# Optimization experiments

Hardware: AMD Instinct MI355X
Metric: run time of the kernel (lower is better)

## Reference

```python
import jax, jax.numpy as jnp
import numpy as np

B, N, C = 256, 196, 256
RES, RES_, STRIDE = 14, 7, 2
H, KD, D = 16, 16, 64          # heads, key_dim, d=attn_ratio*key_dim
NH_KD, DH = H * KD, H * D      # 256, 1024
HW = DH + NH_KD                # kv width 1280
OUT = 512
EPS = 1e-5
SCALE = KD ** -0.5


def make_bias_idxs():
    pts = [(i, j) for i in range(RES) for j in range(RES)]
    pts_ = [(i, j) for i in range(RES_) for j in range(RES_)]
    offsets, idxs = {}, []
    for p1 in pts_:
        for p2 in pts:
            off = (abs(p1[0] * STRIDE - p2[0]), abs(p1[1] * STRIDE - p2[1]))
            if off not in offsets:
                offsets[off] = len(offsets)
            idxs.append(offsets[off])
    return np.array(idxs, np.int32).reshape(len(pts_), len(pts)), len(offsets)


def bn(x, g, b, m, v):
    return (x - m) * (g / jnp.sqrt(v + EPS)) + b


def hardswish(x):
    return x * jnp.clip(x + 3.0, 0.0, 6.0) / 6.0


def setup_inputs() -> dict:
    key = jax.random.key(0)
    ks = jax.random.split(key, 12)
    idxs, n_off = make_bias_idxs()
    s_in, s_dh = (2.0 / C) ** 0.5, (2.0 / DH) ** 0.5
    return {
        "x": jax.random.normal(ks[0], (B, N, C), jnp.float32),
        "W_kv": jax.random.normal(ks[1], (HW, C), jnp.float32) * s_in,
        "g_kv": jnp.ones((HW,)), "b_kv": jnp.zeros((HW,)),
        "m_kv": jax.random.normal(ks[2], (HW,)) * 0.1,
        "v_kv": jax.random.uniform(ks[3], (HW,), minval=0.5, maxval=1.5),
        "W_q": jax.random.normal(ks[4], (NH_KD, C), jnp.float32) * s_in,
        "g_q": jnp.ones((NH_KD,)), "b_q": jnp.zeros((NH_KD,)),
        "m_q": jax.random.normal(ks[5], (NH_KD,)) * 0.1,
        "v_q": jax.random.uniform(ks[6], (NH_KD,), minval=0.5, maxval=1.5),
        "W_p": jax.random.normal(ks[7], (OUT, DH), jnp.float32) * s_dh,
        "g_p": jnp.ones((OUT,)), "b_p": jnp.zeros((OUT,)),
        "m_p": jax.random.normal(ks[8], (OUT,)) * 0.1,
        "v_p": jax.random.uniform(ks[9], (OUT,), minval=0.5, maxval=1.5),
        "attn_biases": jax.random.normal(ks[10], (H, n_off), jnp.float32) * 0.02,
        "bias_idxs": jnp.asarray(idxs),
    }


def reference(x, W_kv, g_kv, b_kv, m_kv, v_kv, W_q, g_q, b_q, m_q, v_q,
              W_p, g_p, b_p, m_p, v_p, attn_biases, bias_idxs):
    # kv branch: Linear(no bias) + BN over flattened tokens
    kv = bn(jnp.einsum('bnc,hc->bnh', x, W_kv), g_kv, b_kv, m_kv, v_kv)
    kv = kv.reshape(B, N, H, KD + D)
    k, v = kv[..., :KD], kv[..., KD:]                 # [B,N,H,KD], [B,N,H,D]
    # q branch: spatial subsample stride 2 then LinearNorm
    xs = x.reshape(B, RES, RES, C)[:, ::STRIDE, ::STRIDE].reshape(B, RES_ * RES_, C)
    q = bn(jnp.einsum('bnc,hc->bnh', xs, W_q), g_q, b_q, m_q, v_q)
    q = q.reshape(B, RES_ * RES_, H, KD)              # [B,49,H,KD]
    bias = attn_biases[:, bias_idxs]                  # [H,49,196]
    attn = jnp.einsum('bqhd,bkhd->bhqk', q, k) * SCALE + bias
    attn = jax.nn.softmax(attn, axis=-1)
    o = jnp.einsum('bhqk,bkhd->bqhd', attn, v).reshape(B, RES_ * RES_, DH)
    return bn(jnp.einsum('bnd,od->bno', hardswish(o), W_p), g_p, b_p, m_p, v_p)
```

## Files before the change

kernel.cpp:

```cpp
#include <hip/hip_runtime.h>

typedef unsigned short u16;
typedef unsigned int u32;
typedef __attribute__((ext_vector_type(8))) short bf16x8;
typedef __attribute__((ext_vector_type(4))) float f32x4;

__device__ __forceinline__ u16 f2bf(float x) {
  union { float f; u32 u; } un; un.f = x;
  u32 r = un.u + 0x7FFFu + ((un.u >> 16) & 1u);
  return (u16)(r >> 16);
}

__device__ __forceinline__ void gl_lds16(const u16* gsrc, u16* ldst) {
  __builtin_amdgcn_global_load_lds(
      (const __attribute__((address_space(1))) void*)gsrc,
      (__attribute__((address_space(3))) void*)ldst,
      16, 0, 0);
}

__global__ __launch_bounds__(256) void prep_misc(
    const float* __restrict__ Wkv, const float* __restrict__ Wq, const float* __restrict__ Wp,
    const float* __restrict__ gkv, const float* __restrict__ bkv, const float* __restrict__ mkv, const float* __restrict__ vkv,
    const float* __restrict__ gq, const float* __restrict__ bq, const float* __restrict__ mq, const float* __restrict__ vq,
    const float* __restrict__ gp, const float* __restrict__ bp, const float* __restrict__ mp, const float* __restrict__ vp,
    const float* __restrict__ ab, const int* __restrict__ bidx,
    u16* __restrict__ wkvb, u16* __restrict__ wqb, u16* __restrict__ wpb,
    float* __restrict__ skv, float* __restrict__ tkv,
    float* __restrict__ sq, float* __restrict__ tq,
    float* __restrict__ sp, float* __restrict__ tp,
    float* __restrict__ biasf)
{
  int i = blockIdx.x * 256 + threadIdx.x;
  if (i < 327680) { wkvb[i] = f2bf(Wkv[i]); return; }
  i -= 327680;
  if (i < 65536) { wqb[i] = f2bf(Wq[i]); return; }
  i -= 65536;
  if (i < 524288) { wpb[i] = f2bf(Wp[i]); return; }
  i -= 524288;
  if (i < 153664) { biasf[i] = ab[(i / 9604) * 196 + bidx[i % 9604]]; return; }
  i -= 153664;
  if (i < 1280) { float s = gkv[i] * rsqrtf(vkv[i] + 1e-5f); skv[i] = s; tkv[i] = bkv[i] - mkv[i] * s; return; }
  i -= 1280;
  if (i < 256) { float s = gq[i] * rsqrtf(vq[i] + 1e-5f); sq[i] = s * 0.25f; tq[i] = (bq[i] - mq[i] * s) * 0.25f; return; }
  i -= 256;
  if (i < 512) { float s = gp[i] * rsqrtf(vp[i] + 1e-5f); sp[i] = s; tp[i] = bp[i] - mp[i] * s; return; }
}

__global__ __launch_bounds__(256) void conv_x(const float* __restrict__ x, u16* __restrict__ xb)
{
  int u = blockIdx.x * 256 + threadIdx.x;
  float4 v = ((const float4*)x)[u];
  uint2 o;
  o.x = (u32)f2bf(v.x) | ((u32)f2bf(v.y) << 16);
  o.y = (u32)f2bf(v.z) | ((u32)f2bf(v.w) << 16);
  ((uint2*)xb)[u] = o;
}

__global__ __launch_bounds__(256) void gemm_bn(
    const u16* __restrict__ A, const u16* __restrict__ W,
    const float* __restrict__ sv, const float* __restrict__ tv,
    float* __restrict__ outp, int N, int K, int NBLK)
{
  __shared__ u16 As[128 * 64];
  __shared__ u16 Bs[128 * 64];
  const int tid = threadIdx.x;
  const int lane = tid & 63;
  const int wv = tid >> 6, wr = wv >> 1, wc = wv & 1;
  const int lo = lane & 15, hi = lane >> 4;

  int bid = blockIdx.x;
  int cpx = gridDim.x >> 3;
  int wg = (bid & 7) * cpx + (bid >> 3);
  const int m0 = (wg / NBLK) * 128, n0 = (wg % NBLK) * 128;

  f32x4 zero4 = {0.f, 0.f, 0.f, 0.f};
  f32x4 acc[4][4];
#pragma unroll
  for (int m = 0; m < 4; ++m)
#pragma unroll
    for (int n = 0; n < 4; ++n) acc[m][n] = zero4;

  for (int kt = 0; kt < K; kt += 64) {
    __syncthreads();
#pragma unroll
    for (int i = 0; i < 4; ++i) {
      int e = (i * 256 + tid) * 8;
      int r = e >> 6, c = e & 63;
      int cs = c ^ ((r & 7) << 3);
      gl_lds16(A + (long)(m0 + r) * K + (kt + cs), As + e);
      gl_lds16(W + (long)(n0 + r) * K + (kt + cs), Bs + e);
    }
    __syncthreads();
#pragma unroll
    for (int kk = 0; kk < 64; kk += 32) {
      bf16x8 af[4], bfr[4];
#pragma unroll
      for (int m = 0; m < 4; ++m)
        af[m] = *(const bf16x8*)(As + (wr * 64 + m * 16 + lo) * 64 + ((kk + hi * 8) ^ ((lo & 7) << 3)));
#pragma unroll
      for (int n = 0; n < 4; ++n)
        bfr[n] = *(const bf16x8*)(Bs + (wc * 64 + n * 16 + lo) * 64 + ((kk + hi * 8) ^ ((lo & 7) << 3)));
#pragma unroll
      for (int m = 0; m < 4; ++m)
#pragma unroll
        for (int n = 0; n < 4; ++n)
          acc[m][n] = __builtin_amdgcn_mfma_f32_16x16x32_bf16(af[m], bfr[n], acc[m][n], 0, 0, 0);
    }
  }
#pragma unroll
  for (int m = 0; m < 4; ++m) {
    const int row0 = m0 + wr * 64 + m * 16 + hi * 4;
#pragma unroll
    for (int n = 0; n < 4; ++n) {
      const int col = n0 + wc * 64 + n * 16 + lo;
      const float s = sv[col], t = tv[col];
#pragma unroll
      for (int j = 0; j < 4; ++j)
        outp[(long)(row0 + j) * N + col] = acc[m][n][j] * s + t;
    }
  }
}

#define WOFF  13312
#define VTS   208
#define KOFF  13312
#define KS    24
#define QOFF  18304
#define QS    24
#define POFF  13312
#define PS    208
#define SMEM_N 26624

__device__ __forceinline__ int swz(int col, int rowkey) {
  return (col < 192) ? (col ^ ((rowkey & 7) << 3)) : col;
}

__global__ __launch_bounds__(256, 3) void fused_attn(
    const u16* __restrict__ xb, const u16* __restrict__ wkvb, const u16* __restrict__ wqb,
    const float* __restrict__ skv, const float* __restrict__ tkv,
    const float* __restrict__ sqv, const float* __restrict__ tqv,
    const float* __restrict__ biasf, u16* __restrict__ osw)
{
  __shared__ __align__(16) u16 sm[SMEM_N];
  const int tid = threadIdx.x;
  const int bid = blockIdx.x;
  const int wg = (bid & 7) * 512 + (bid >> 3);
  const int bb = wg >> 4, hh = wg & 15;
  const int w = tid >> 6, lane = tid & 63, lo = lane & 15, hi = lane >> 4;

  const u16* xbase = xb + (long)bb * 196 * 256;
  const u16* wkvh = wkvb + (long)hh * 80 * 256;
  const u16* wqh  = wqb + (long)hh * 16 * 256;

  const int NM = (w == 0) ? 4 : 3;
  f32x4 z4 = {0.f, 0.f, 0.f, 0.f};
  f32x4 acc[4][5];
#pragma unroll
  for (int u = 0; u < 4; ++u)
#pragma unroll
    for (int nf = 0; nf < 5; ++nf) acc[u][nf] = z4;
  f32x4 qacc = z4;

  int qi = w * 16 + lo; if (qi > 48) qi = 48;
  const int gr = (qi / 7) * 28 + (qi % 7) * 2;

  for (int kt = 0; kt < 256; kt += 64) {
    __syncthreads();
#pragma unroll
    for (int i = 0; i < 7; ++i) {
      if (i < 6 || tid < 128) {
        int e = (i * 256 + tid) * 8;
        int r = e >> 6, c = e & 63;
        int xr = (r < 196) ? r : 195;
        int cs = c ^ ((r & 7) << 3);
        gl_lds16(xbase + (long)xr * 256 + kt + cs, sm + e);
      }
    }
#pragma unroll
    for (int i = 0; i < 3; ++i) {
      int e = (i * 256 + tid) * 8;
      int r = e >> 6, c = e & 63;
      int cs = c ^ ((r & 7) << 3);
      const u16* src = (r < 80) ? (wkvh + (long)r * 256 + kt + cs)
                                : (wqh + (long)(r - 80) * 256 + kt + cs);
      gl_lds16(src, sm + WOFF + e);
    }
    __syncthreads();
    __builtin_amdgcn_s_setprio(1);
#pragma unroll
    for (int kk = 0; kk < 64; kk += 32) {
      bf16x8 bfr[6];
#pragma unroll
      for (int nf = 0; nf < 6; ++nf)
        bfr[nf] = *(const bf16x8*)(sm + WOFF + (nf * 16 + lo) * 64 + ((kk + hi * 8) ^ ((lo & 7) << 3)));
      {
        bf16x8 aqf = *(const bf16x8*)(sm + gr * 64 + ((kk + hi * 8) ^ ((gr & 7) << 3)));
        qacc = __builtin_amdgcn_mfma_f32_16x16x32_bf16(aqf, bfr[5], qacc, 0, 0, 0);
      }
#pragma unroll
      for (int u = 0; u < 4; ++u) {
        if (u < NM) {
          const int mf = w + u * 4;
          bf16x8 af = *(const bf16x8*)(sm + (mf * 16 + lo) * 64 + ((kk + hi * 8) ^ ((lo & 7) << 3)));
#pragma unroll
          for (int nf = 0; nf < 5; ++nf)
            acc[u][nf] = __builtin_amdgcn_mfma_f32_16x16x32_bf16(af, bfr[nf], acc[u][nf], 0, 0, 0);
        }
      }
    }
    __builtin_amdgcn_s_setprio(0);
  }
  __syncthreads();

#pragma unroll
  for (int u = 0; u < 4; ++u) {
    if (u < NM) {
      const int mf = w + u * 4;
#pragma unroll
      for (int nf = 0; nf < 5; ++nf) {
        const int col = nf * 16 + lo;
        const float s = skv[hh * 80 + col], t = tkv[hh * 80 + col];
#pragma unroll
        for (int j = 0; j < 4; ++j) {
          const int nn = mf * 16 + hi * 4 + j;
          const u16 bv = f2bf(acc[u][nf][j] * s + t);
          if (col < 16) sm[KOFF + nn * KS + col] = bv;
          else          sm[(col - 16) * VTS + swz(nn, col - 16)] = bv;
        }
      }
    }
  }
  {
    const float s = sqv[hh * 16 + lo], t = tqv[hh * 16 + lo];
#pragma unroll
    for (int j = 0; j < 4; ++j) {
      const int r = w * 16 + hi * 4 + j;
      sm[QOFF + r * QS + lo] = f2bf(qacc[j] * s + t);
    }
  }
  __syncthreads();

  f32x4 sc[13];
  {
    bf16x8 zf = {0, 0, 0, 0, 0, 0, 0, 0};
    bf16x8 aq2 = zf;
    if (hi < 2) aq2 = *(const bf16x8*)(sm + QOFF + (w * 16 + lo) * QS + hi * 8);
#pragma unroll
    for (int t13 = 0; t13 < 13; ++t13) {
      bf16x8 bk = zf;
      if (hi < 2) bk = *(const bf16x8*)(sm + KOFF + (t13 * 16 + lo) * KS + hi * 8);
      sc[t13] = __builtin_amdgcn_mfma_f32_16x16x32_bf16(aq2, bk, z4, 0, 0, 0);
    }
  }
  __syncthreads();

  float rs[4];
#pragma unroll
  for (int j = 0; j < 4; ++j) {
    const int row = w * 16 + hi * 4 + j;
    const int rb = (row < 49) ? row : 0;
    float vals[13];
#pragma unroll
    for (int t = 0; t < 13; ++t) {
      const int col = t * 16 + lo;
      vals[t] = (col < 196) ? sc[t][j] + biasf[(hh * 49 + rb) * 196 + col] : -1e30f;
    }
    float mx = vals[0];
#pragma unroll
    for (int t = 1; t < 13; ++t) mx = fmaxf(mx, vals[t]);
#pragma unroll
    for (int s = 1; s < 16; s <<= 1) mx = fmaxf(mx, __shfl_xor(mx, s, 64));
    float sum = 0.f;
#pragma unroll
    for (int t = 0; t < 13; ++t) { float p = __expf(vals[t] - mx); vals[t] = p; sum += p; }
#pragma unroll
    for (int s = 1; s < 16; s <<= 1) sum += __shfl_xor(sum, s, 64);
#pragma unroll
    for (int t = 0; t < 13; ++t) sm[POFF + row * PS + swz(t * 16 + lo, row)] = f2bf(vals[t]);
    rs[j] = sum;
  }

  f32x4 oacc[4];
#pragma unroll
  for (int n = 0; n < 4; ++n) oacc[n] = z4;
  __builtin_amdgcn_s_setprio(1);
#pragma unroll
  for (int kt = 0; kt < 192; kt += 32) {
    bf16x8 ap = *(const bf16x8*)(sm + POFF + (w * 16 + lo) * PS + ((kt + hi * 8) ^ ((lo & 7) << 3)));
#pragma unroll
    for (int n = 0; n < 4; ++n) {
      bf16x8 bv = *(const bf16x8*)(sm + (n * 16 + lo) * VTS + ((kt + hi * 8) ^ ((lo & 7) << 3)));
      oacc[n] = __builtin_amdgcn_mfma_f32_16x16x32_bf16(ap, bv, oacc[n], 0, 0, 0);
    }
  }
  {
    bf16x8 zf = {0, 0, 0, 0, 0, 0, 0, 0};
    bf16x8 ap = zf;
    if (hi < 2) ap = *(const bf16x8*)(sm + POFF + (w * 16 + lo) * PS + 192 + hi * 8);
#pragma unroll
    for (int n = 0; n < 4; ++n) {
      bf16x8 bv = zf;
      if (hi < 2) bv = *(const bf16x8*)(sm + (n * 16 + lo) * VTS + 192 + hi * 8);
      oacc[n] = __builtin_amdgcn_mfma_f32_16x16x32_bf16(ap, bv, oacc[n], 0, 0, 0);
    }
  }
  __builtin_amdgcn_s_setprio(0);

#pragma unroll
  for (int j = 0; j < 4; ++j) {
    const int row = w * 16 + hi * 4 + j;
    if (row < 49) {
      const float rinv = 1.f / rs[j];
      const long ob = ((long)(bb * 49 + row)) * 1024 + hh * 64 + lo;
#pragma unroll
      for (int n = 0; n < 4; ++n) {
        float val = oacc[n][j] * rinv;
        float hs = val * fminf(fmaxf(val + 3.f, 0.f), 6.f) * (1.f / 6.f);
        osw[ob + n * 16] = f2bf(hs);
      }
    }
  }
}

extern "C" void kernel_launch(void* const* d_in, const int* in_sizes, int n_in,
                              void* d_out, int out_size, void* d_ws, size_t ws_size,
                              hipStream_t stream)
{
  const float* x   = (const float*)d_in[0];
  const float* Wkv = (const float*)d_in[1];
  const float* gkv = (const float*)d_in[2];
  const float* bkv = (const float*)d_in[3];
  const float* mkv = (const float*)d_in[4];
  const float* vkv = (const float*)d_in[5];
  const float* Wq  = (const float*)d_in[6];
  const float* gq  = (const float*)d_in[7];
  const float* bq  = (const float*)d_in[8];
  const float* mq  = (const float*)d_in[9];
  const float* vq  = (const float*)d_in[10];
  const float* Wp  = (const float*)d_in[11];
  const float* gp  = (const float*)d_in[12];
  const float* bp  = (const float*)d_in[13];
  const float* mp  = (const float*)d_in[14];
  const float* vp  = (const float*)d_in[15];
  const float* ab  = (const float*)d_in[16];
  const int* bidx  = (const int*)d_in[17];

  char* ws = (char*)d_ws;
  size_t off = 0;
  auto alloc = [&](size_t bytes) -> char* {
    char* p = ws + off;
    off += (bytes + 255) & ~(size_t)255;
    return p;
  };
  u16* x_bf   = (u16*)alloc((size_t)50176 * 256 * 2);
  u16* wkv_bf = (u16*)alloc((size_t)1280 * 256 * 2);
  u16* wq_bf  = (u16*)alloc((size_t)256 * 256 * 2);
  u16* wp_bf  = (u16*)alloc((size_t)512 * 1024 * 2);
  u16* hsw    = (u16*)alloc((size_t)12544 * 1024 * 2);
  float* bias_f = (float*)alloc((size_t)153664 * 4);
  float* s_kv = (float*)alloc(1280 * 4);
  float* t_kv = (float*)alloc(1280 * 4);
  float* s_q  = (float*)alloc(256 * 4);
  float* t_q  = (float*)alloc(256 * 4);
  float* s_p  = (float*)alloc(512 * 4);
  float* t_p  = (float*)alloc(512 * 4);
  if (off > ws_size) return;

  prep_misc<<<4193, 256, 0, stream>>>(Wkv, Wq, Wp, gkv, bkv, mkv, vkv,
                                      gq, bq, mq, vq, gp, bp, mp, vp,
                                      ab, bidx, wkv_bf, wq_bf, wp_bf,
                                      s_kv, t_kv, s_q, t_q, s_p, t_p, bias_f);
  conv_x<<<12544, 256, 0, stream>>>(x, x_bf);
  fused_attn<<<4096, 256, 0, stream>>>(x_bf, wkv_bf, wq_bf, s_kv, t_kv, s_q, t_q, bias_f, hsw);
  gemm_bn<<<392, 256, 0, stream>>>(hsw, wp_bf, s_p, t_p, (float*)d_out, 512, 1024, 4);
}
```

Baseline: 126.2 us.

## Fold K/V batch-norm into q scale and output, rebalance last KV tile

```diff
diff --git a/kernel.cpp b/kernel.cpp
--- a/kernel.cpp
+++ b/kernel.cpp
@@ -41,7 +41,14 @@
   i -= 153664;
   if (i < 1280) { float s = gkv[i] * rsqrtf(vkv[i] + 1e-5f); skv[i] = s; tkv[i] = bkv[i] - mkv[i] * s; return; }
   i -= 1280;
-  if (i < 256) { float s = gq[i] * rsqrtf(vq[i] + 1e-5f); sq[i] = s * 0.25f; tq[i] = (bq[i] - mq[i] * s) * 0.25f; return; }
+  if (i < 256) {
+    int h = i >> 4, c = i & 15;
+    float sk = gkv[h * 80 + c] * rsqrtf(vkv[h * 80 + c] + 1e-5f);
+    float s = gq[i] * rsqrtf(vq[i] + 1e-5f);
+    sq[i] = s * 0.25f * sk;
+    tq[i] = (bq[i] - mq[i] * s) * 0.25f * sk;
+    return;
+  }
   i -= 256;
   if (i < 512) { float s = gp[i] * rsqrtf(vp[i] + 1e-5f); sp[i] = s; tp[i] = bp[i] - mp[i] * s; return; }
 }
@@ -152,13 +159,13 @@
   const u16* wkvh = wkvb + (long)hh * 80 * 256;
   const u16* wqh  = wqb + (long)hh * 16 * 256;
 
-  const int NM = (w == 0) ? 4 : 3;
   f32x4 z4 = {0.f, 0.f, 0.f, 0.f};
-  f32x4 acc[4][5];
-#pragma unroll
-  for (int u = 0; u < 4; ++u)
+  f32x4 acc[3][5];
+#pragma unroll
+  for (int u = 0; u < 3; ++u)
 #pragma unroll
     for (int nf = 0; nf < 5; ++nf) acc[u][nf] = z4;
+  f32x4 acc12a = z4, acc12b = z4;
   f32x4 qacc = z4;
 
   int qi = w * 16 + lo; if (qi > 48) qi = 48;
@@ -189,22 +196,33 @@
     __builtin_amdgcn_s_setprio(1);
 #pragma unroll
     for (int kk = 0; kk < 64; kk += 32) {
+      const int csw = (kk + hi * 8) ^ ((lo & 7) << 3);
       bf16x8 bfr[6];
 #pragma unroll
       for (int nf = 0; nf < 6; ++nf)
-        bfr[nf] = *(const bf16x8*)(sm + WOFF + (nf * 16 + lo) * 64 + ((kk + hi * 8) ^ ((lo & 7) << 3)));
+        bfr[nf] = *(const bf16x8*)(sm + WOFF + (nf * 16 + lo) * 64 + csw);
       {
         bf16x8 aqf = *(const bf16x8*)(sm + gr * 64 + ((kk + hi * 8) ^ ((gr & 7) << 3)));
         qacc = __builtin_amdgcn_mfma_f32_16x16x32_bf16(aqf, bfr[5], qacc, 0, 0, 0);
       }
 #pragma unroll
-      for (int u = 0; u < 4; ++u) {
-        if (u < NM) {
-          const int mf = w + u * 4;
-          bf16x8 af = *(const bf16x8*)(sm + (mf * 16 + lo) * 64 + ((kk + hi * 8) ^ ((lo & 7) << 3)));
-#pragma unroll
-          for (int nf = 0; nf < 5; ++nf)
-            acc[u][nf] = __builtin_amdgcn_mfma_f32_16x16x32_bf16(af, bfr[nf], acc[u][nf], 0, 0, 0);
+      for (int u = 0; u < 3; ++u) {
+        const int mf = w + u * 4;
+        bf16x8 af = *(const bf16x8*)(sm + (mf * 16 + lo) * 64 + csw);
+#pragma unroll
+        for (int nf = 0; nf < 5; ++nf)
+          acc[u][nf] = __builtin_amdgcn_mfma_f32_16x16x32_bf16(af, bfr[nf], acc[u][nf], 0, 0, 0);
+      }
+      if (w) {
+        bf16x8 af12 = *(const bf16x8*)(sm + (192 + lo) * 64 + csw);
+        if (w == 1) {
+          acc12a = __builtin_amdgcn_mfma_f32_16x16x32_bf16(af12, bfr[0], acc12a, 0, 0, 0);
+          acc12b = __builtin_amdgcn_mfma_f32_16x16x32_bf16(af12, bfr[1], acc12b, 0, 0, 0);
+        } else if (w == 2) {
+          acc12a = __builtin_amdgcn_mfma_f32_16x16x32_bf16(af12, bfr[2], acc12a, 0, 0, 0);
+          acc12b = __builtin_amdgcn_mfma_f32_16x16x32_bf16(af12, bfr[3], acc12b, 0, 0, 0);
+        } else {
+          acc12a = __builtin_amdgcn_mfma_f32_16x16x32_bf16(af12, bfr[4], acc12a, 0, 0, 0);
         }
       }
     }
@@ -213,21 +231,47 @@
   __syncthreads();
 
 #pragma unroll
-  for (int u = 0; u < 4; ++u) {
-    if (u < NM) {
-      const int mf = w + u * 4;
-#pragma unroll
-      for (int nf = 0; nf < 5; ++nf) {
-        const int col = nf * 16 + lo;
-        const float s = skv[hh * 80 + col], t = tkv[hh * 80 + col];
-#pragma unroll
-        for (int j = 0; j < 4; ++j) {
-          const int nn = mf * 16 + hi * 4 + j;
-          const u16 bv = f2bf(acc[u][nf][j] * s + t);
-          if (col < 16) sm[KOFF + nn * KS + col] = bv;
-          else          sm[(col - 16) * VTS + swz(nn, col - 16)] = bv;
-        }
-      }
+  for (int u = 0; u < 3; ++u) {
+    const int mf = w + u * 4;
+    const int nnb = mf * 16 + hi * 4;
+#pragma unroll
+    for (int j = 0; j < 4; ++j)
+      sm[KOFF + (nnb + j) * KS + lo] = f2bf(acc[u][0][j]);
+#pragma unroll
+    for (int nf = 1; nf < 5; ++nf) {
+      const int d = nf * 16 - 16 + lo;
+      uint2 pp;
+      pp.x = (u32)f2bf(acc[u][nf][0]) | ((u32)f2bf(acc[u][nf][1]) << 16);
+      pp.y = (u32)f2bf(acc[u][nf][2]) | ((u32)f2bf(acc[u][nf][3]) << 16);
+      *(uint2*)(sm + d * VTS + swz(nnb, d)) = pp;
+    }
+  }
+  {
+    const int nnb = 192 + hi * 4;
+    if (w == 1) {
+#pragma unroll
+      for (int j = 0; j < 4; ++j)
+        sm[KOFF + (nnb + j) * KS + lo] = f2bf(acc12a[j]);
+      const int d = lo;
+      uint2 pp;
+      pp.x = (u32)f2bf(acc12b[0]) | ((u32)f2bf(acc12b[1]) << 16);
+      pp.y = (u32)f2bf(acc12b[2]) | ((u32)f2bf(acc12b[3]) << 16);
+      *(uint2*)(sm + d * VTS + swz(nnb, d)) = pp;
+    } else if (w == 2) {
+      const int d0 = 16 + lo, d1 = 32 + lo;
+      uint2 pa, pb;
+      pa.x = (u32)f2bf(acc12a[0]) | ((u32)f2bf(acc12a[1]) << 16);
+      pa.y = (u32)f2bf(acc12a[2]) | ((u32)f2bf(acc12a[3]) << 16);
+      pb.x = (u32)f2bf(acc12b[0]) | ((u32)f2bf(acc12b[1]) << 16);
+      pb.y = (u32)f2bf(acc12b[2]) | ((u32)f2bf(acc12b[3]) << 16);
+      *(uint2*)(sm + d0 * VTS + swz(nnb, d0)) = pa;
+      *(uint2*)(sm + d1 * VTS + swz(nnb, d1)) = pb;
+    } else if (w == 3) {
+      const int d = 48 + lo;
+      uint2 pp;
+      pp.x = (u32)f2bf(acc12a[0]) | ((u32)f2bf(acc12a[1]) << 16);
+      pp.y = (u32)f2bf(acc12a[2]) | ((u32)f2bf(acc12a[3]) << 16);
+      *(uint2*)(sm + d * VTS + swz(nnb, d)) = pp;
     }
   }
   {
@@ -306,6 +350,12 @@
   }
   __builtin_amdgcn_s_setprio(0);
 
+  float svv[4], tvv[4];
+#pragma unroll
+  for (int n = 0; n < 4; ++n) {
+    svv[n] = skv[hh * 80 + 16 + n * 16 + lo];
+    tvv[n] = tkv[hh * 80 + 16 + n * 16 + lo];
+  }
 #pragma unroll
   for (int j = 0; j < 4; ++j) {
     const int row = w * 16 + hi * 4 + j;
@@ -314,7 +364,7 @@
       const long ob = ((long)(bb * 49 + row)) * 1024 + hh * 64 + lo;
 #pragma unroll
       for (int n = 0; n < 4; ++n) {
-        float val = oacc[n][j] * rinv;
+        float val = oacc[n][j] * svv[n] * rinv + tvv[n];
         float hs = val * fminf(fmaxf(val + 3.f, 0.f), 6.f) * (1.f / 6.f);
         osw[ob + n * 16] = f2bf(hs);
       }
```

After: 125.7 us. About the same (-0.4%).
